# Performance work log

Hardware: AMD Instinct MI355X
Metric: run time of the kernel (lower is better)

The kernel has to match this reference:

```python
import jax, jax.numpy as jnp
import numpy as np

H = 2048   # hidden_size
NH = 32    # n_head
HS = 64    # head_size
B, T = 2, 4096
D_DECAY, D_AAA, D_MV, D_GATE = 96, 96, 64, 256


def setup_inputs() -> dict:
    key = jax.random.key(0)
    ks = jax.random.split(key, 30)
    rn = lambda k, s, sc=0.02: jax.random.normal(k, s, jnp.float32) * sc
    d = {}
    d['x'] = jax.random.normal(ks[0], (B, T, H), jnp.float32)
    d['shift_state_in'] = jax.random.normal(ks[1], (B, H), jnp.float32)
    d['wkv_state_in'] = jnp.zeros((B, NH, HS, HS), jnp.float32)
    d['v_first_val'] = jax.random.normal(ks[2], (B, T, H), jnp.float32)
    for i, n in enumerate(['x_r', 'x_w', 'x_k', 'x_v', 'x_a', 'x_g']):
        d[n] = jax.random.uniform(ks[3 + i], (H,), jnp.float32)
    d['w0'] = rn(ks[9], (H,)) - 4.0
    d['w1'] = rn(ks[10], (H, D_DECAY)); d['w2'] = rn(ks[11], (D_DECAY, H))
    d['a0'] = rn(ks[12], (H,)); d['a1'] = rn(ks[13], (H, D_AAA)); d['a2'] = rn(ks[14], (D_AAA, H))
    d['v0'] = rn(ks[15], (H,)) + 1.0; d['v1'] = rn(ks[16], (H, D_MV)); d['v2'] = rn(ks[17], (D_MV, H))
    d['g1'] = rn(ks[18], (H, D_GATE)); d['g2'] = rn(ks[19], (D_GATE, H))
    d['k_k'] = jnp.full((H,), 0.85, jnp.float32)
    d['k_a'] = jnp.ones((H,), jnp.float32)
    d['r_k'] = rn(ks[20], (NH, HS))
    s = 1.0 / np.sqrt(H)
    d['W_r'] = jax.random.normal(ks[21], (H, H), jnp.float32) * s
    d['W_k'] = jax.random.normal(ks[22], (H, H), jnp.float32) * s
    d['W_v'] = jax.random.normal(ks[23], (H, H), jnp.float32) * s
    d['W_o'] = jax.random.normal(ks[24], (H, H), jnp.float32) * s
    d['ln_w'] = jnp.ones((H,), jnp.float32)
    d['ln_b'] = jnp.zeros((H,), jnp.float32)
    return d


def _forward(x, shift_state_in, wkv_state_in, v_first_val, x_r, x_w, x_k, x_v, x_a, x_g,
             w0, w1, w2, a0, a1, a2, v0, v1, v2, g1, g2, k_k, k_a, r_k,
             W_r, W_k, W_v, W_o, ln_w, ln_b):
    Bx, Tx, C = x.shape
    # token shift: previous token embedding (shift_state for t=0)
    xprev = jnp.concatenate([shift_state_in[:, None, :], x[:, :-1]], axis=1)
    dx = xprev - x
    xr, xw, xk, xv, xa, xg = (x + dx * m for m in (x_r, x_w, x_k, x_v, x_a, x_g))
    r = xr @ W_r.T
    k = xk @ W_k.T
    v = xv @ W_v.T
    # soft-clamped log-decay (<= -0.5)
    w_raw = -jax.nn.softplus(-(w0 + jnp.tanh(xw @ w1) @ w2)) - 0.5
    # layer_id > 0: residual mix with first-layer value
    v = v + (v_first_val - v) * jax.nn.sigmoid(v0 + (xv @ v1) @ v2)
    a = jax.nn.sigmoid(a0 + (xa @ a1) @ a2)          # in-context learning rate
    g = jax.nn.sigmoid(xg @ g1) @ g2                 # output gate
    kk = (k * k_k).reshape(Bx, Tx, NH, HS)
    kk = kk / jnp.maximum(jnp.linalg.norm(kk, axis=-1, keepdims=True), 1e-12)  # F.normalize
    kk = kk.reshape(Bx, Tx, C)
    k = k * (1.0 + (a - 1.0) * k_a)
    w = jnp.exp(-jnp.exp(w_raw))                     # per-channel decay in (0,1)
    heads = lambda t: t.reshape(Bx, Tx, NH, HS).transpose(1, 0, 2, 3)  # [T,B,NH,HS]
    rs, ws, ks_, vs, kks, as_ = map(heads, (r, w, k, v, kk, a))

    def step(S, inp):
        # S: [B,NH,HS(value),HS(key)]
        rt, wt, kt, vt, kkt, at = inp
        sa = jnp.einsum('bhvk,bhk->bhv', S, -kkt)
        S = (S * wt[:, :, None, :]
             + sa[:, :, :, None] * (kkt * at)[:, :, None, :]
             + vt[:, :, :, None] * kt[:, :, None, :])
        return S, jnp.einsum('bhvk,bhk->bhv', S, rt)

    wkv_state_out, y = jax.lax.scan(step, wkv_state_in, (rs, ws, ks_, vs, kks, as_))
    y = y.transpose(1, 0, 2, 3)                      # [B,T,NH,HS]
    # GroupNorm(n_head groups, eps=1e-5*head_size)
    mu = y.mean(-1, keepdims=True)
    var = y.var(-1, keepdims=True)
    y = ((y - mu) / jnp.sqrt(var + 1e-5 * HS)).reshape(Bx, Tx, C) * ln_w + ln_b
    rk = (r.reshape(Bx, Tx, NH, HS) * k.reshape(Bx, Tx, NH, HS) * r_k).sum(-1, keepdims=True)
    y = y + (rk * v.reshape(Bx, Tx, NH, HS)).reshape(Bx, Tx, C)
    out = (y * g) @ W_o.T
    return out, x[:, -1], wkv_state_out, v_first_val


def reference(x, shift_state_in, wkv_state_in, v_first_val, x_r, x_w, x_k, x_v, x_a, x_g,
              w0, w1, w2, a0, a1, a2, v0, v1, v2, g1, g2, k_k, k_a, r_k,
              W_r, W_k, W_v, W_o, ln_w, ln_b):
    return _forward(x, shift_state_in, wkv_state_in, v_first_val, x_r, x_w, x_k, x_v, x_a, x_g,
                    w0, w1, w2, a0, a1, a2, v0, v1, v2, g1, g2, k_k, k_a, r_k,
                    W_r, W_k, W_v, W_o, ln_w, ln_b)
```

## Files before the change

### kernel.cpp

```cpp
#include <hip/hip_runtime.h>

typedef unsigned short u16;
typedef __attribute__((ext_vector_type(4))) float f32x4;
typedef __attribute__((ext_vector_type(8))) __bf16 bf16x8;
typedef __attribute__((ext_vector_type(8))) unsigned short u16x8;
typedef __attribute__((ext_vector_type(4))) unsigned short u16x4;

#define DI static __device__ __forceinline__

DI float bfu2f(u16 u){ unsigned int x = ((unsigned int)u)<<16; float f; __builtin_memcpy(&f,&x,4); return f; }
DI u16 f2bfu(float f){ __bf16 h = (__bf16)f; u16 u; __builtin_memcpy(&u,&h,2); return u; }
DI float sigm(float x){ return 1.f/(1.f+expf(-x)); }

DI void gload_lds16(const void* g, void* l) {
  __builtin_amdgcn_global_load_lds(
      (const __attribute__((address_space(1))) unsigned int*)g,
      (__attribute__((address_space(3))) unsigned int*)l, 16, 0, 0);
}

template<bool OBF16>
__global__ __launch_bounds__(256) void gemm128_k(
    const u16* __restrict__ A, const u16* __restrict__ Bt,
    void* __restrict__ Cp, int M, int N, int K)
{
  __shared__ alignas(16) u16 As[128*64];
  __shared__ alignas(16) u16 Bs[128*64];
  const int tid = threadIdx.x;
  const int wid = tid >> 6, lane = tid & 63;
  const int wm = wid >> 1, wn = wid & 1;
  const int l15 = lane & 15, q = lane >> 4;
  const int m0 = blockIdx.x * 128, n0 = blockIdx.y * 128;
  const int sr = (wid << 3) + (lane >> 3);
  const int sc = (lane & 7) << 3;
  f32x4 acc[4][4];
  #pragma unroll
  for (int i=0;i<4;i++)
    #pragma unroll
    for (int j=0;j<4;j++) acc[i][j] = f32x4{0.f,0.f,0.f,0.f};

  char* la = (char*)As + (size_t)wid*1024;
  char* lb = (char*)Bs + (size_t)wid*1024;
  for (int k0 = 0; k0 < K; k0 += 64) {
    const u16* ga = A  + (size_t)(m0 + sr)*K + k0 + sc;
    const u16* gb = Bt + (size_t)(n0 + sr)*K + k0 + sc;
    #pragma unroll
    for (int it = 0; it < 4; ++it) {
      gload_lds16(ga + (size_t)(32*it)*K, la + it*4096);
      gload_lds16(gb + (size_t)(32*it)*K, lb + it*4096);
    }
    __syncthreads();
    #pragma unroll
    for (int ks = 0; ks < 64; ks += 32) {
      bf16x8 af[4], bfv[4];
      #pragma unroll
      for (int i=0;i<4;i++) af[i]  = *(const bf16x8*)&As[(wm*64 + i*16 + l15)*64 + ks + q*8];
      #pragma unroll
      for (int j=0;j<4;j++) bfv[j] = *(const bf16x8*)&Bs[(wn*64 + j*16 + l15)*64 + ks + q*8];
      #pragma unroll
      for (int i=0;i<4;i++)
        #pragma unroll
        for (int j=0;j<4;j++)
          acc[i][j] = __builtin_amdgcn_mfma_f32_16x16x32_bf16(af[i], bfv[j], acc[i][j], 0, 0, 0);
    }
    __syncthreads();
  }
  #pragma unroll
  for (int i=0;i<4;i++)
    #pragma unroll
    for (int j=0;j<4;j++)
      #pragma unroll
      for (int rr=0;rr<4;rr++) {
        const int gm = m0 + wm*64 + i*16 + q*4 + rr;
        const int gn = n0 + wn*64 + j*16 + l15;
        const size_t o = (size_t)gm * (size_t)N + gn;
        if constexpr (OBF16) ((u16*)Cp)[o] = f2bfu(acc[i][j][rr]);
        else                 ((float*)Cp)[o] = acc[i][j][rr];
      }
}

constexpr int LDW = 72;

template<bool MIX, bool WNK, bool ABF16, bool OBF16, int EPI=0>
__global__ __launch_bounds__(256) void gemm_k(
    const void* __restrict__ Ap, const float* __restrict__ dxp, const float* __restrict__ mixp,
    const float* __restrict__ Wp, void* __restrict__ Cp, int M, int N, int K)
{
  __shared__ alignas(16) __bf16 As[64*LDW];
  __shared__ alignas(16) __bf16 Bs[64*LDW];
  const int tid = threadIdx.x;
  const int m0 = blockIdx.x * 64;
  const int n0 = blockIdx.y * 64;
  const int lane = tid & 63, wid = tid >> 6;
  const int wm = wid >> 1, wn = wid & 1;
  const int l15 = lane & 15, q = lane >> 4;
  f32x4 acc[2][2] = {{{0.f,0.f,0.f,0.f},{0.f,0.f,0.f,0.f}},
                     {{0.f,0.f,0.f,0.f},{0.f,0.f,0.f,0.f}}};

  for (int k0 = 0; k0 < K; k0 += 64) {
    {
      const int kc = (tid & 7) * 8;
      const int r0 = tid >> 3;
      #pragma unroll
      for (int it = 0; it < 2; ++it) {
        const int row = r0 + 32*it;
        const size_t gmK = (size_t)(m0 + row) * (size_t)K;
        const int gk = k0 + kc;
        if constexpr (ABF16) {
          const u16* A16 = (const u16*)Ap;
          u16x8 u;
          if (gk + 7 < K) u = *(const u16x8*)(A16 + gmK + gk);
          else {
            #pragma unroll
            for (int e=0;e<8;e++) u[e] = (gk+e < K) ? A16[gmK + gk + e] : (u16)0;
          }
          *(u16x8*)&As[row*LDW + kc] = u;
        } else {
          const float* A32 = (const float*)Ap;
          float f[8];
          if (gk + 7 < K) {
            f32x4 va = *(const f32x4*)(A32 + gmK + gk);
            f32x4 vb = *(const f32x4*)(A32 + gmK + gk + 4);
            if constexpr (MIX) {
              f32x4 d0 = *(const f32x4*)(dxp + gmK + gk);
              f32x4 d1 = *(const f32x4*)(dxp + gmK + gk + 4);
              f32x4 c0 = *(const f32x4*)(mixp + gk);
              f32x4 c1 = *(const f32x4*)(mixp + gk + 4);
              va = va + d0*c0; vb = vb + d1*c1;
            }
            #pragma unroll
            for (int e=0;e<4;e++){ f[e]=va[e]; f[4+e]=vb[e]; }
          } else {
            #pragma unroll
            for (int e=0;e<8;e++){
              const int kk2 = gk+e;
              float xv = 0.f;
              if (kk2 < K) {
                xv = A32[gmK + kk2];
                if constexpr (MIX) xv = fmaf(dxp[gmK+kk2], mixp[kk2], xv);
              }
              f[e] = xv;
            }
          }
          bf16x8 v8;
          #pragma unroll
          for (int e=0;e<8;e++) v8[e] = (__bf16)f[e];
          *(bf16x8*)&As[row*LDW + kc] = v8;
        }
      }
    }
    if constexpr (WNK) {
      const int kc = (tid & 7) * 8;
      const int r0 = tid >> 3;
      #pragma unroll
      for (int it = 0; it < 2; ++it) {
        const int row = r0 + 32*it;
        const int gn = n0 + row;
        const int gk = k0 + kc;
        float f[8];
        if (gn < N && gk + 7 < K) {
          const size_t o = (size_t)gn * (size_t)K + gk;
          f32x4 va = *(const f32x4*)(Wp + o);
          f32x4 vb = *(const f32x4*)(Wp + o + 4);
          #pragma unroll
          for (int e=0;e<4;e++){ f[e]=va[e]; f[4+e]=vb[e]; }
        } else {
          #pragma unroll
          for (int e=0;e<8;e++) f[e] = (gn < N && gk+e < K) ? Wp[(size_t)gn*K + gk + e] : 0.f;
        }
        bf16x8 v8;
        #pragma unroll
        for (int e=0;e<8;e++) v8[e] = (__bf16)f[e];
        *(bf16x8*)&Bs[row*LDW + kc] = v8;
      }
    } else {
      const int nc = (tid & 15) * 4;
      const int kr = tid >> 4;
      #pragma unroll
      for (int it = 0; it < 4; ++it) {
        const int kk = kr + 16*it;
        const int gk = k0 + kk;
        f32x4 v = {0.f,0.f,0.f,0.f};
        if (gk < K) {
          const int gn = n0 + nc;
          if (gn + 3 < N) v = *(const f32x4*)(Wp + (size_t)gk*N + gn);
          else {
            #pragma unroll
            for (int e=0;e<4;e++) if (gn+e < N) v[e] = Wp[(size_t)gk*N + gn + e];
          }
        }
        #pragma unroll
        for (int e=0;e<4;e++) Bs[(nc+e)*LDW + kk] = (__bf16)v[e];
      }
    }
    __syncthreads();
    #pragma unroll
    for (int ks = 0; ks < 64; ks += 32) {
      bf16x8 af[2], bfv[2];
      #pragma unroll
      for (int i=0;i<2;i++) af[i]  = *(const bf16x8*)&As[(wm*32 + i*16 + l15)*LDW + ks + q*8];
      #pragma unroll
      for (int i=0;i<2;i++) bfv[i] = *(const bf16x8*)&Bs[(wn*32 + i*16 + l15)*LDW + ks + q*8];
      #pragma unroll
      for (int i=0;i<2;i++)
        #pragma unroll
        for (int j=0;j<2;j++)
          acc[i][j] = __builtin_amdgcn_mfma_f32_16x16x32_bf16(af[i], bfv[j], acc[i][j], 0, 0, 0);
    }
    __syncthreads();
  }
  #pragma unroll
  for (int i=0;i<2;i++) {
    #pragma unroll
    for (int j=0;j<2;j++) {
      #pragma unroll
      for (int rr=0;rr<4;rr++) {
        const int gm = m0 + wm*32 + i*16 + q*4 + rr;
        const int gn = n0 + wn*32 + j*16 + l15;
        if (gn < N) {
          const size_t o = (size_t)gm * (size_t)N + gn;
          if constexpr (EPI == 1) {
            float* C = (float*)Cp;
            const float s = sigm(mixp[gn] + acc[i][j][rr]);
            const float vG = C[o];
            C[o] = vG + (dxp[o] - vG) * s;
          } else if constexpr (OBF16) {
            ((u16*)Cp)[o] = f2bfu(acc[i][j][rr]);
          } else {
            ((float*)Cp)[o] = acc[i][j][rr];
          }
        }
      }
    }
  }
}

__global__ void mix_cast_k(const float* __restrict__ x, const float* __restrict__ shift,
    const float* __restrict__ mr, const float* __restrict__ mw, const float* __restrict__ mk,
    const float* __restrict__ mv, const float* __restrict__ ma, const float* __restrict__ mg,
    u16* __restrict__ xr_b, u16* __restrict__ xw_b, u16* __restrict__ xk_b,
    u16* __restrict__ xv_b, u16* __restrict__ xa_b, u16* __restrict__ xg_b,
    float* __restrict__ xlast, int T_, int B_)
{
  const int Hh = 2048;
  size_t e4 = (size_t)blockIdx.x*blockDim.x + threadIdx.x;
  size_t total4 = (size_t)B_*T_*Hh/4;
  if (e4 >= total4) return;
  size_t e = e4*4;
  size_t th = (size_t)T_*Hh;
  size_t b = e / th; size_t rem = e - b*th;
  int t = (int)(rem / Hh); int c = (int)(rem & (Hh-1));
  f32x4 xv4 = *(const f32x4*)(x+e);
  f32x4 xp = t ? *(const f32x4*)(x+e-Hh) : *(const f32x4*)(shift + b*Hh + c);
  f32x4 dx = xp - xv4;
  if (t == T_-1) *(f32x4*)(xlast + b*Hh + c) = xv4;
  #define EMIT(mp, dst) { \
    f32x4 mc = *(const f32x4*)(mp + c); \
    f32x4 r_ = xv4 + dx*mc; \
    u16x4 o_; \
    o_[0]=f2bfu(r_[0]); o_[1]=f2bfu(r_[1]); o_[2]=f2bfu(r_[2]); o_[3]=f2bfu(r_[3]); \
    *(u16x4*)(dst + e) = o_; }
  EMIT(mr, xr_b) EMIT(mw, xw_b) EMIT(mk, xk_b)
  EMIT(mv, xv_b) EMIT(ma, xa_b) EMIT(mg, xg_b)
  #undef EMIT
}

__global__ void castw_k(const float* __restrict__ src, u16* __restrict__ dst, long n4){
  long i = (long)blockIdx.x*blockDim.x + threadIdx.x;
  if (i < n4) {
    f32x4 v = ((const f32x4*)src)[i];
    u16x4 o; o[0]=f2bfu(v[0]); o[1]=f2bfu(v[1]); o[2]=f2bfu(v[2]); o[3]=f2bfu(v[3]);
    ((u16x4*)dst)[i] = o;
  }
}

__global__ void ew_tanh_k(u16* p, long n){
  long i = (long)blockIdx.x*blockDim.x + threadIdx.x;
  if (i < n) p[i] = f2bfu(tanhf(bfu2f(p[i])));
}
__global__ void ew_sig_k(u16* p, long n){
  long i = (long)blockIdx.x*blockDim.x + threadIdx.x;
  if (i < n) p[i] = f2bfu(sigm(bfu2f(p[i])));
}
__global__ void ew_w_k(float* p, const float* __restrict__ w0, long n){
  long i = (long)blockIdx.x*blockDim.x + threadIdx.x;
  if (i < n) {
    int c = (int)(i & 2047);
    float z = -(w0[c] + p[i]);
    float sp = (z > 20.f) ? z : log1pf(expf(z));
    p[i] = expf(-expf(-sp - 0.5f));
  }
}
__global__ void ew_a_k(u16* p, const float* __restrict__ a0, long n){
  long i = (long)blockIdx.x*blockDim.x + threadIdx.x;
  if (i < n) { int c = (int)(i & 2047); p[i] = f2bfu(sigm(a0[c] + bfu2f(p[i]))); }
}
__global__ void copy4_k(float* __restrict__ dst, const float* __restrict__ src, long n4){
  long i = (long)blockIdx.x*blockDim.x + threadIdx.x;
  if (i < n4) ((f32x4*)dst)[i] = ((const f32x4*)src)[i];
}

__global__ __launch_bounds__(256) void rnorm_k(
    const u16* __restrict__ kb, const float* __restrict__ kkw, float* __restrict__ r2)
{
  const size_t bt = blockIdx.x;
  const int tid = threadIdx.x;
  const int c0 = tid << 3;
  u16x8 kv8 = *(const u16x8*)(kb + bt*2048 + c0);
  f32x4 ka_ = *(const f32x4*)(kkw + c0);
  f32x4 kb_ = *(const f32x4*)(kkw + c0 + 4);
  float s = 0.f;
  #pragma unroll
  for (int e=0;e<4;e++){ float kk = bfu2f(kv8[e])*ka_[e];   s = fmaf(kk,kk,s); }
  #pragma unroll
  for (int e=0;e<4;e++){ float kk = bfu2f(kv8[4+e])*kb_[e]; s = fmaf(kk,kk,s); }
  s += __shfl_xor(s, 1, 64);
  s += __shfl_xor(s, 2, 64);
  s += __shfl_xor(s, 4, 64);
  if ((tid & 7) == 0) r2[bt*32 + (tid>>3)] = 1.f/fmaxf(s, 1e-24f);
}

__global__ __launch_bounds__(64) __attribute__((amdgpu_waves_per_eu(1, 4)))
void scan_k(
    const u16* __restrict__ rb, const float* __restrict__ wb, const u16* __restrict__ kb,
    const float* __restrict__ vb, const u16* __restrict__ ab,
    const float* __restrict__ kkw, const float* __restrict__ kaw,
    const float* __restrict__ S0, float* __restrict__ yb, float* __restrict__ Sout, int T_)
{
  const int Hh = 2048, NHl = 32;
  const int blk = blockIdx.x;
  const int b = blk >> 5, h = blk & 31;
  const int lane = threadIdx.x;
  float S[64];
  const size_t sbase = (((size_t)b*NHl + h)*64 + lane)*64;
  #pragma unroll
  for (int i=0;i<64;i++) S[i] = S0[sbase+i];
  const float kkc = kkw[h*64+lane], kac = kaw[h*64+lane];
  __shared__ alignas(16) float lw[64], lkk[64], lka[64], lke[64], lr[64];
  size_t idx = (size_t)b*T_*Hh + (size_t)h*64 + lane;
  float rv = bfu2f(rb[idx]), wv = wb[idx], kv = bfu2f(kb[idx]), vv = vb[idx], av = bfu2f(ab[idx]);
  for (int t=0; t<T_; ++t) {
    float kk = kv * kkc;
    float ssum = kk*kk;
    #pragma unroll
    for (int m=1;m<64;m<<=1) ssum += __shfl_xor(ssum, m, 64);
    float inv = 1.f / fmaxf(sqrtf(ssum), 1e-12f);
    float kkn = kk * inv;
    float ke  = kv * (1.f + (av - 1.f)*kac);
    lw[lane]=wv; lkk[lane]=kkn; lka[lane]=kkn*av; lke[lane]=ke; lr[lane]=rv;
    const float vt = vv;
    __syncthreads();
    float nrv=0.f,nwv=0.f,nkv=0.f,nvv=0.f,nav=0.f;
    if (t+1 < T_) {
      const size_t ni = idx + Hh;
      nrv = bfu2f(rb[ni]); nwv = wb[ni]; nkv = bfu2f(kb[ni]); nvv = vb[ni]; nav = bfu2f(ab[ni]);
    }
    const f32x4* KK4 = (const f32x4*)lkk;
    const f32x4* W4  = (const f32x4*)lw;
    const f32x4* KA4 = (const f32x4*)lka;
    const f32x4* KE4 = (const f32x4*)lke;
    const f32x4* R4  = (const f32x4*)lr;
    float sa0=0.f,sa1=0.f,sa2=0.f,sa3=0.f;
    #pragma unroll
    for (int qq=0;qq<16;qq++){
      f32x4 k4 = KK4[qq];
      sa0 = fmaf(S[4*qq+0], k4[0], sa0);
      sa1 = fmaf(S[4*qq+1], k4[1], sa1);
      sa2 = fmaf(S[4*qq+2], k4[2], sa2);
      sa3 = fmaf(S[4*qq+3], k4[3], sa3);
    }
    const float sa = -((sa0+sa1)+(sa2+sa3));
    float y0=0.f,y1=0.f,y2=0.f,y3=0.f;
    #pragma unroll
    for (int qq=0;qq<16;qq++){
      f32x4 w4=W4[qq], a4=KA4[qq], e4=KE4[qq], r4=R4[qq];
      float s_;
      s_ = fmaf(vt, e4[0], fmaf(sa, a4[0], S[4*qq+0]*w4[0])); S[4*qq+0]=s_; y0 = fmaf(s_, r4[0], y0);
      s_ = fmaf(vt, e4[1], fmaf(sa, a4[1], S[4*qq+1]*w4[1])); S[4*qq+1]=s_; y1 = fmaf(s_, r4[1], y1);
      s_ = fmaf(vt, e4[2], fmaf(sa, a4[2], S[4*qq+2]*w4[2])); S[4*qq+2]=s_; y2 = fmaf(s_, r4[2], y2);
      s_ = fmaf(vt, e4[3], fmaf(sa, a4[3], S[4*qq+3]*w4[3])); S[4*qq+3]=s_; y3 = fmaf(s_, r4[3], y3);
    }
    yb[idx] = (y0+y1)+(y2+y3);
    __syncthreads();
    rv=nrv; wv=nwv; kv=nkv; vv=nvv; av=nav;
    idx += Hh;
  }
  #pragma unroll
  for (int i=0;i<64;i++) Sout[sbase+i] = S[i];
}

__global__ __launch_bounds__(256) void chunk_mu_k(
    const u16* __restrict__ rb, const float* __restrict__ wb, const u16* __restrict__ kb,
    const float* __restrict__ vb, const u16* __restrict__ ab,
    const float* __restrict__ kkw, const float* __restrict__ kaw,
    const float* __restrict__ r2b,
    float* __restrict__ Mbuf, float* __restrict__ Ubuf, float* __restrict__ Dbuf,
    float* __restrict__ yb, int T_, int NC)
{
  const int wid  = threadIdx.x >> 6;
  const int lane = threadIdx.x & 63;
  const int g    = blockIdx.x * 4 + wid;
  const int ch   = g >> 1;
  const bool mrole = ((g & 1) == 0);
  const int c  = ch % NC;
  const int bh = ch / NC;
  const int b = bh >> 5, h = bh & 31;

  float S[64];
  #pragma unroll
  for (int i=0;i<64;i++) S[i] = (mrole && lane == i) ? 1.f : 0.f;

  const int hc = h*64 + lane;
  const float kkc = kkw[hc], kac = kaw[hc];

  __shared__ alignas(16) float LB[4][2][5][64];
  float (*Lw)[5][64] = LB[wid];

  size_t idx = ((size_t)b*T_ + (size_t)c*64)*2048 + hc;
  size_t r2i = ((size_t)b*T_ + (size_t)c*64)*32 + h;
  float* dD = Dbuf + (size_t)ch*4096 + lane;

  {
    const float kv = bfu2f(kb[idx]);
    const float av = bfu2f(ab[idx]);
    const float kk = kv*kkc;
    Lw[0][0][lane] = wb[idx];
    Lw[0][1][lane] = kk;
    Lw[0][2][lane] = kk*av;
    Lw[0][3][lane] = kv*(1.f+(av-1.f)*kac);
    Lw[0][4][lane] = bfu2f(rb[idx]);
  }
  float vv = mrole ? 0.f : vb[idx];
  float r2 = r2b[r2i];

  for (int j=0; j<64; ++j) {
    const int cur = j & 1;
    float nr=0.f,nk=0.f,nw=0.f,na=0.f,nv=0.f,nr2=0.f;
    if (j+1 < 64) {
      const size_t ni = idx + 2048;
      nr = bfu2f(rb[ni]); nk = bfu2f(kb[ni]); nw = wb[ni]; na = bfu2f(ab[ni]);
      if (!mrole) nv = vb[ni];
      nr2 = r2b[r2i + 32];
    }
    const f32x4* W4  = (const f32x4*)Lw[cur][0];
    const f32x4* KK4 = (const f32x4*)Lw[cur][1];
    const f32x4* KA4 = (const f32x4*)Lw[cur][2];
    const f32x4* KE4 = (const f32x4*)Lw[cur][3];
    const f32x4* R4  = (const f32x4*)Lw[cur][4];
    float s0=0.f,s1=0.f,s2=0.f,s3=0.f;
    #pragma unroll
    for (int qq=0;qq<16;qq++){
      f32x4 k4 = KK4[qq];
      s0 = fmaf(S[4*qq+0], k4[0], s0);
      s1 = fmaf(S[4*qq+1], k4[1], s1);
      s2 = fmaf(S[4*qq+2], k4[2], s2);
      s3 = fmaf(S[4*qq+3], k4[3], s3);
    }
    const float sa = -((s0+s1)+(s2+s3)) * r2;
    const float vt = vv;
    float y0=0.f,y1=0.f,y2=0.f,y3=0.f;
    if (mrole) {
      #pragma unroll
      for (int qq=0;qq<16;qq++){
        f32x4 w4=W4[qq], a4=KA4[qq], r4=R4[qq];
        float s_;
        s_ = fmaf(sa, a4[0], S[4*qq+0]*w4[0]); S[4*qq+0]=s_; y0 = fmaf(s_, r4[0], y0);
        s_ = fmaf(sa, a4[1], S[4*qq+1]*w4[1]); S[4*qq+1]=s_; y1 = fmaf(s_, r4[1], y1);
        s_ = fmaf(sa, a4[2], S[4*qq+2]*w4[2]); S[4*qq+2]=s_; y2 = fmaf(s_, r4[2], y2);
        s_ = fmaf(sa, a4[3], S[4*qq+3]*w4[3]); S[4*qq+3]=s_; y3 = fmaf(s_, r4[3], y3);
      }
      dD[(size_t)j*64] = (y0+y1)+(y2+y3);
    } else {
      #pragma unroll
      for (int qq=0;qq<16;qq++){
        f32x4 w4=W4[qq], a4=KA4[qq], e4=KE4[qq], r4=R4[qq];
        float s_;
        s_ = fmaf(vt, e4[0], fmaf(sa, a4[0], S[4*qq+0]*w4[0])); S[4*qq+0]=s_; y0 = fmaf(s_, r4[0], y0);
        s_ = fmaf(vt, e4[1], fmaf(sa, a4[1], S[4*qq+1]*w4[1])); S[4*qq+1]=s_; y1 = fmaf(s_, r4[1], y1);
        s_ = fmaf(vt, e4[2], fmaf(sa, a4[2], S[4*qq+2]*w4[2])); S[4*qq+2]=s_; y2 = fmaf(s_, r4[2], y2);
        s_ = fmaf(vt, e4[3], fmaf(sa, a4[3], S[4*qq+3]*w4[3])); S[4*qq+3]=s_; y3 = fmaf(s_, r4[3], y3);
      }
      yb[idx] = (y0+y1)+(y2+y3);
    }
    if (j+1 < 64) {
      const float kk = nk*kkc;
      Lw[cur^1][0][lane] = nw;
      Lw[cur^1][1][lane] = kk;
      Lw[cur^1][2][lane] = kk*na;
      Lw[cur^1][3][lane] = nk*(1.f+(na-1.f)*kac);
      Lw[cur^1][4][lane] = nr;
    }
    vv = nv; r2 = nr2;
    idx += 2048; r2i += 32;
  }
  float* fd = (mrole ? Mbuf : Ubuf) + (size_t)ch*4096 + (size_t)lane*64;
  #pragma unroll
  for (int qq=0;qq<16;qq++)
    *(f32x4*)(fd + 4*qq) = f32x4{S[4*qq+0],S[4*qq+1],S[4*qq+2],S[4*qq+3]};
}

__global__ __launch_bounds__(256) void propagate_k(
    const float* __restrict__ Mbuf, const float* Ubuf,
    const float* __restrict__ S0, float* SSbuf, float* __restrict__ Sout, int NC)
{
  const int bh   = blockIdx.x >> 2;
  const int v0r  = (blockIdx.x & 3) * 16;
  const int tid  = threadIdx.x;
  const int lane = tid & 63;
  const int wvv  = tid >> 6;

  __shared__ float MT[64*65];
  __shared__ float Srow[16][64];

  #pragma unroll
  for (int i=0;i<4;i++) {
    const int v = v0r + wvv*4 + i;
    Srow[wvv*4+i][lane] = S0[((size_t)bh*64 + v)*64 + lane];
  }

  const size_t mbase = (size_t)bh * NC * 4096;
  f32x4 mreg[4];
  #pragma unroll
  for (int it=0; it<4; ++it)
    mreg[it] = *(const f32x4*)(Mbuf + mbase + it*1024 + tid*4);

  for (int c=0; c<NC; ++c) {
    const size_t chB = mbase + (size_t)c*4096;
    #pragma unroll
    for (int it=0; it<4; ++it) {
      const int base = it*1024 + tid*4;
      const int j = base >> 6;
      const int k = base & 63;
      #pragma unroll
      for (int e=0;e<4;e++) MT[(k+e)*65 + j] = mreg[it][e];
    }
    __syncthreads();
    if (c+1 < NC) {
      #pragma unroll
      for (int it=0; it<4; ++it)
        mreg[it] = *(const f32x4*)(Mbuf + chB + 4096 + it*1024 + tid*4);
    }
    float u[4];
    #pragma unroll
    for (int i=0;i<4;i++)
      u[i] = Ubuf[chB + (size_t)(v0r + wvv*4 + i)*64 + lane];
    #pragma unroll
    for (int i=0;i<4;i++)
      SSbuf[chB + (size_t)(v0r + wvv*4 + i)*64 + lane] = Srow[wvv*4+i][lane];
    float acc[4] = {0.f,0.f,0.f,0.f};
    #pragma unroll
    for (int j4=0; j4<16; ++j4) {
      float m0_ = MT[lane*65 + j4*4 + 0];
      float m1_ = MT[lane*65 + j4*4 + 1];
      float m2_ = MT[lane*65 + j4*4 + 2];
      float m3_ = MT[lane*65 + j4*4 + 3];
      #pragma unroll
      for (int i=0;i<4;i++) {
        f32x4 s4 = *(const f32x4*)&Srow[wvv*4+i][j4*4];
        acc[i] = fmaf(s4[0], m0_, acc[i]);
        acc[i] = fmaf(s4[1], m1_, acc[i]);
        acc[i] = fmaf(s4[2], m2_, acc[i]);
        acc[i] = fmaf(s4[3], m3_, acc[i]);
      }
    }
    #pragma unroll
    for (int i=0;i<4;i++) Srow[wvv*4+i][lane] = acc[i] + u[i];
    __syncthreads();
  }
  #pragma unroll
  for (int i=0;i<4;i++) {
    const int v = v0r + wvv*4 + i;
    Sout[((size_t)bh*64 + v)*64 + lane] = Srow[wvv*4+i][lane];
  }
}

__global__ __launch_bounds__(64) void ycorr_k(
    const float* __restrict__ SSbuf, const float* __restrict__ Dbuf,
    float* __restrict__ yb, int T_, int NC)
{
  const int ch = blockIdx.x;
  const int c  = ch % NC;
  const int bh = ch / NC;
  const int b = bh >> 5, h = bh & 31;
  const int lane = threadIdx.x;

  __shared__ alignas(16) float Dl[64*68];

  {
    const float* sg = SSbuf + (size_t)ch*4096;
    #pragma unroll
    for (int i=0;i<16;i++){
      const int o = i*256 + lane*4;
      f32x4 v = *(const f32x4*)(sg + o);
      *(f32x4*)&Dl[(o>>6)*68 + (o&63)] = v;
    }
  }
  __syncthreads();
  float ss[64];
  #pragma unroll
  for (int qq=0;qq<16;qq++){
    f32x4 v = *(const f32x4*)&Dl[lane*68 + 4*qq];
    ss[4*qq+0]=v[0]; ss[4*qq+1]=v[1]; ss[4*qq+2]=v[2]; ss[4*qq+3]=v[3];
  }
  __syncthreads();
  {
    const float* dg = Dbuf + (size_t)ch*4096;
    #pragma unroll
    for (int i=0;i<16;i++){
      const int o = i*256 + lane*4;
      f32x4 v = *(const f32x4*)(dg + o);
      *(f32x4*)&Dl[(o>>6)*68 + (o&63)] = v;
    }
  }
  __syncthreads();

  size_t idx = ((size_t)b*T_ + (size_t)c*64)*2048 + (size_t)h*64 + lane;
  for (int t=0; t<64; ++t) {
    const f32x4* D4 = (const f32x4*)&Dl[t*68];
    float a0=0.f,a1=0.f,a2=0.f,a3=0.f;
    #pragma unroll
    for (int qq=0;qq<16;qq++){
      f32x4 d4 = D4[qq];
      a0 = fmaf(ss[4*qq+0], d4[0], a0);
      a1 = fmaf(ss[4*qq+1], d4[1], a1);
      a2 = fmaf(ss[4*qq+2], d4[2], a2);
      a3 = fmaf(ss[4*qq+3], d4[3], a3);
    }
    yb[idx] = yb[idx] + ((a0+a1)+(a2+a3));
    idx += 2048;
  }
}

__global__ __launch_bounds__(256) void post_k(
    const float* __restrict__ yb, const u16* __restrict__ rb, const u16* __restrict__ kb,
    const u16* __restrict__ ab, const u16* __restrict__ gb, const float* __restrict__ vb,
    const float* __restrict__ kaw, const float* __restrict__ rkw,
    const float* __restrict__ lnw, const float* __restrict__ lnb, u16* __restrict__ zb)
{
  const int wid = threadIdx.x >> 6, lane = threadIdx.x & 63;
  const size_t unit = (size_t)blockIdx.x*4 + wid;
  const size_t bt = unit >> 5; const int h = (int)(unit & 31);
  const size_t idx = bt*2048 + (size_t)h*64 + lane;
  const int hc = h*64 + lane;
  const float yv = yb[idx];
  const float rv = bfu2f(rb[idx]), kv = bfu2f(kb[idx]), av = bfu2f(ab[idx]);
  const float ke = kv*(1.f + (av-1.f)*kaw[hc]);
  float s1 = yv, s2 = yv*yv, rk = rv*ke*rkw[hc];
  #pragma unroll
  for (int m=1;m<64;m<<=1){
    s1 += __shfl_xor(s1,m,64);
    s2 += __shfl_xor(s2,m,64);
    rk += __shfl_xor(rk,m,64);
  }
  const float mean = s1 * (1.f/64.f);
  const float var  = s2 * (1.f/64.f) - mean*mean;
  const float rstd = rsqrtf(var + 6.4e-4f);
  const float zn = (yv-mean)*rstd*lnw[hc] + lnb[hc] + rk*vb[idx];
  zb[idx] = f2bfu(zn * bfu2f(gb[idx]));
}

extern "C" void kernel_launch(void* const* d_in, const int* in_sizes, int n_in,
                              void* d_out, int out_size, void* d_ws, size_t ws_size,
                              hipStream_t stream)
{
  const float* x      = (const float*)d_in[0];
  const float* shift  = (const float*)d_in[1];
  const float* wkv0   = (const float*)d_in[2];
  const float* vfirst = (const float*)d_in[3];
  const float* xr = (const float*)d_in[4];
  const float* xw = (const float*)d_in[5];
  const float* xk = (const float*)d_in[6];
  const float* xv = (const float*)d_in[7];
  const float* xa = (const float*)d_in[8];
  const float* xg = (const float*)d_in[9];
  const float* w0 = (const float*)d_in[10];
  const float* w1 = (const float*)d_in[11];
  const float* w2 = (const float*)d_in[12];
  const float* a0 = (const float*)d_in[13];
  const float* a1 = (const float*)d_in[14];
  const float* a2 = (const float*)d_in[15];
  const float* v0 = (const float*)d_in[16];
  const float* v1 = (const float*)d_in[17];
  const float* v2 = (const float*)d_in[18];
  const float* g1 = (const float*)d_in[19];
  const float* g2 = (const float*)d_in[20];
  const float* k_k = (const float*)d_in[21];
  const float* k_a = (const float*)d_in[22];
  const float* r_k = (const float*)d_in[23];
  const float* W_r = (const float*)d_in[24];
  const float* W_k = (const float*)d_in[25];
  const float* W_v = (const float*)d_in[26];
  const float* W_o = (const float*)d_in[27];
  const float* ln_w = (const float*)d_in[28];
  const float* ln_b = (const float*)d_in[29];

  const int H = 2048, NH = 32;
  const int BH = in_sizes[1];
  const int B  = BH / H;
  const long BTH = (long)in_sizes[0];
  const int T  = (int)(BTH / BH);
  const int M  = (int)(BTH / H);

  float* out0 = (float*)d_out;
  float* out1 = out0 + BTH;
  float* out2 = out1 + BH;
  float* out3 = out2 + (size_t)B*NH*64*64;

  char* ws = (char*)d_ws;
  u16* mixb = (u16*)ws;  ws += (size_t)BTH*12;
  u16* xr_b = mixb + 0*BTH;
  u16* xw_b = mixb + 1*BTH;
  u16* xk_b = mixb + 2*BTH;
  u16* xv_b = mixb + 3*BTH;
  u16* xa_b = mixb + 4*BTH;
  u16* xg_b = mixb + 5*BTH;
  float* Mbuf  = (float*)mixb;
  float* Ubuf  = Mbuf + BTH;
  float* Dbuf  = Ubuf + BTH;
  float* SSbuf = Ubuf;
  u16*   zb16  = (u16*)mixb;
  u16* rb   = (u16*)ws;  ws += BTH*2;
  u16* kb   = (u16*)ws;  ws += BTH*2;
  u16* ab   = (u16*)ws;  ws += BTH*2;
  u16* gb   = (u16*)ws;  ws += BTH*2;
  u16* wr16 = (u16*)ws;  ws += (size_t)H*H*2;
  u16* wk16 = (u16*)ws;  ws += (size_t)H*H*2;
  u16* wv16 = (u16*)ws;  ws += (size_t)H*H*2;
  u16* wo16 = (u16*)ws;  ws += (size_t)H*H*2;
  u16* h1w  = (u16*)ws;  ws += (size_t)M*96*2;
  u16* h1a  = (u16*)ws;  ws += (size_t)M*96*2;
  u16* h1v  = (u16*)ws;  ws += (size_t)M*64*2;
  u16* h1g  = (u16*)ws;  ws += (size_t)M*256*2;
  float* dxz = (float*)ws; ws += BTH*4;
  float* r2b = (float*)h1w;
  const size_t ws_need = (size_t)(ws - (char*)d_ws);
  const bool chunked = (ws_size >= ws_need) && (T % 64 == 0);
  const bool big_ok  = (M % 128 == 0);
  (void)n_in; (void)out_size;

  const dim3 blk(256);
  auto gg  = [&](int N){ return dim3(M/64, (N+63)/64); };
  auto gg128 = [&](int N){ return dim3(M/128, N/128); };

  mix_cast_k<<<dim3((unsigned)((BTH/4 + 255)/256)), blk, 0, stream>>>(
      x, shift, xr, xw, xk, xv, xa, xg, xr_b, xw_b, xk_b, xv_b, xa_b, xg_b, out1, T, B);

  {
    const long n4 = (long)H*H/4;
    const dim3 gw((unsigned)((n4 + 255)/256));
    castw_k<<<gw, blk, 0, stream>>>(W_r, wr16, n4);
    castw_k<<<gw, blk, 0, stream>>>(W_k, wk16, n4);
    castw_k<<<gw, blk, 0, stream>>>(W_v, wv16, n4);
    castw_k<<<gw, blk, 0, stream>>>(W_o, wo16, n4);
  }

  gemm_k<false,false,true,true><<<gg(96),  blk, 0, stream>>>(xw_b, nullptr, nullptr, w1, h1w, M, 96,  H);
  gemm_k<false,false,true,true><<<gg(96),  blk, 0, stream>>>(xa_b, nullptr, nullptr, a1, h1a, M, 96,  H);
  gemm_k<false,false,true,true><<<gg(64),  blk, 0, stream>>>(xv_b, nullptr, nullptr, v1, h1v, M, 64,  H);
  gemm_k<false,false,true,true><<<gg(256), blk, 0, stream>>>(xg_b, nullptr, nullptr, g1, h1g, M, 256, H);

  ew_tanh_k<<<dim3((unsigned)(((long)M*96 + 255)/256)),  blk, 0, stream>>>(h1w, (long)M*96);
  ew_sig_k <<<dim3((unsigned)(((long)M*256 + 255)/256)), blk, 0, stream>>>(h1g, (long)M*256);

  if (big_ok) {
    gemm128_k<true ><<<gg128(H), blk, 0, stream>>>(xr_b, wr16, rb,   M, H, H);
    gemm128_k<true ><<<gg128(H), blk, 0, stream>>>(xk_b, wk16, kb,   M, H, H);
    gemm128_k<false><<<gg128(H), blk, 0, stream>>>(xv_b, wv16, out3, M, H, H);
  } else {
    gemm_k<false,true,true,true ><<<gg(H), blk, 0, stream>>>(xr_b, nullptr, nullptr, W_r, rb,   M, H, H);
    gemm_k<false,true,true,true ><<<gg(H), blk, 0, stream>>>(xk_b, nullptr, nullptr, W_k, kb,   M, H, H);
    gemm_k<false,true,true,false><<<gg(H), blk, 0, stream>>>(xv_b, nullptr, nullptr, W_v, out3, M, H, H);
  }

  gemm_k<false,false,true,false  ><<<gg(H), blk, 0, stream>>>(h1w, nullptr, nullptr, w2, dxz, M, H, 96);
  rnorm_k<<<dim3((unsigned)M), blk, 0, stream>>>(kb, k_k, r2b);
  gemm_k<false,false,true,true   ><<<gg(H), blk, 0, stream>>>(h1a, nullptr, nullptr, a2, ab,  M, H, 96);
  gemm_k<false,false,true,false,1><<<gg(H), blk, 0, stream>>>(h1v, vfirst,  v0,      v2, out3, M, H, 64);
  gemm_k<false,false,true,true   ><<<gg(H), blk, 0, stream>>>(h1g, nullptr, nullptr, g2, gb,  M, H, 256);

  const unsigned nbB = (unsigned)((BTH + 255)/256);
  ew_w_k<<<dim3(nbB), blk, 0, stream>>>(dxz, w0, BTH);
  ew_a_k<<<dim3(nbB), blk, 0, stream>>>(ab, a0, BTH);

  if (chunked) {
    const int NC = T / 64;
    const int CH = B * NH * NC;
    chunk_mu_k <<<dim3((unsigned)(2*CH/4)), blk, 0, stream>>>(rb, dxz, kb, out3, ab, k_k, k_a, r2b,
                                                              Mbuf, Ubuf, Dbuf, out0, T, NC);
    propagate_k<<<dim3(B*NH*4), blk,       0, stream>>>(Mbuf, Ubuf, wkv0, SSbuf, out2, NC);
    ycorr_k    <<<dim3(CH),     dim3(64),  0, stream>>>(SSbuf, Dbuf, out0, T, NC);
  } else {
    scan_k<<<dim3(B*NH), dim3(64), 0, stream>>>(rb, dxz, kb, out3, ab, k_k, k_a, wkv0, out0, out2, T);
  }

  post_k<<<dim3((unsigned)((size_t)M*NH/4)), blk, 0, stream>>>(out0, rb, kb, ab, gb, out3,
                                                               k_a, r_k, ln_w, ln_b, zb16);

  copy4_k<<<dim3((unsigned)((BTH/4 + 255)/256)), blk, 0, stream>>>(out3, vfirst, BTH/4);

  if (big_ok) {
    gemm128_k<false><<<gg128(H), blk, 0, stream>>>(zb16, wo16, out0, M, H, H);
  } else {
    gemm_k<false,true,true,false><<<gg(H), blk, 0, stream>>>(zb16, nullptr, nullptr, W_o, out0, M, H, H);
  }
}
```

Baseline: 1.956 ms.

## Fuse elementwise activations into GEMM epilogues and triple-buffer chunk scan LDS

Moves the tanh, sigmoid, decay-exp and a-sigmoid elementwise passes into the epilogues of the LoRA GEMMs, removing four separate kernels and their full read/write passes over large intermediate buffers. The chunked scan kernel now uses three LDS buffers and prefetches two timesteps ahead, writing the next step's LDS values before the current step's compute. It also splits the S·kk reduction into more independent accumulators. Fusing the work adds transcendental math to the GEMM epilogues. Writing LDS earlier relies on the three-buffer rotation to avoid a hazard, and the deeper prefetch raises register pressure.

After: 1.893 ms. -3.2%, faster.

```diff
diff --git a/kernel.cpp b/kernel.cpp
--- a/kernel.cpp
+++ b/kernel.cpp
@@ -218,15 +218,26 @@
         const int gn = n0 + wn*32 + j*16 + l15;
         if (gn < N) {
           const size_t o = (size_t)gm * (size_t)N + gn;
+          const float a = acc[i][j][rr];
           if constexpr (EPI == 1) {
             float* C = (float*)Cp;
-            const float s = sigm(mixp[gn] + acc[i][j][rr]);
+            const float s = sigm(mixp[gn] + a);
             const float vG = C[o];
             C[o] = vG + (dxp[o] - vG) * s;
+          } else if constexpr (EPI == 2) {
+            const float z = -(mixp[gn] + a);
+            const float sp = (z > 20.f) ? z : log1pf(expf(z));
+            ((float*)Cp)[o] = expf(-expf(-sp - 0.5f));
+          } else if constexpr (EPI == 3) {
+            ((u16*)Cp)[o] = f2bfu(sigm(mixp[gn] + a));
+          } else if constexpr (EPI == 4) {
+            ((u16*)Cp)[o] = f2bfu(tanhf(a));
+          } else if constexpr (EPI == 5) {
+            ((u16*)Cp)[o] = f2bfu(sigm(a));
           } else if constexpr (OBF16) {
-            ((u16*)Cp)[o] = f2bfu(acc[i][j][rr]);
+            ((u16*)Cp)[o] = f2bfu(a);
           } else {
-            ((float*)Cp)[o] = acc[i][j][rr];
+            ((float*)Cp)[o] = a;
           }
         }
       }
@@ -273,27 +284,6 @@
   }
 }
 
-__global__ void ew_tanh_k(u16* p, long n){
-  long i = (long)blockIdx.x*blockDim.x + threadIdx.x;
-  if (i < n) p[i] = f2bfu(tanhf(bfu2f(p[i])));
-}
-__global__ void ew_sig_k(u16* p, long n){
-  long i = (long)blockIdx.x*blockDim.x + threadIdx.x;
-  if (i < n) p[i] = f2bfu(sigm(bfu2f(p[i])));
-}
-__global__ void ew_w_k(float* p, const float* __restrict__ w0, long n){
-  long i = (long)blockIdx.x*blockDim.x + threadIdx.x;
-  if (i < n) {
-    int c = (int)(i & 2047);
-    float z = -(w0[c] + p[i]);
-    float sp = (z > 20.f) ? z : log1pf(expf(z));
-    p[i] = expf(-expf(-sp - 0.5f));
-  }
-}
-__global__ void ew_a_k(u16* p, const float* __restrict__ a0, long n){
-  long i = (long)blockIdx.x*blockDim.x + threadIdx.x;
-  if (i < n) { int c = (int)(i & 2047); p[i] = f2bfu(sigm(a0[c] + bfu2f(p[i]))); }
-}
 __global__ void copy4_k(float* __restrict__ dst, const float* __restrict__ src, long n4){
   long i = (long)blockIdx.x*blockDim.x + threadIdx.x;
   if (i < n4) ((f32x4*)dst)[i] = ((const f32x4*)src)[i];
@@ -412,7 +402,7 @@
   const int hc = h*64 + lane;
   const float kkc = kkw[hc], kac = kaw[hc];
 
-  __shared__ alignas(16) float LB[4][2][5][64];
+  __shared__ alignas(16) float LB[4][3][5][64];
   float (*Lw)[5][64] = LB[wid];
 
   size_t idx = ((size_t)b*T_ + (size_t)c*64)*2048 + hc;
@@ -429,34 +419,56 @@
     Lw[0][3][lane] = kv*(1.f+(av-1.f)*kac);
     Lw[0][4][lane] = bfu2f(rb[idx]);
   }
-  float vv = mrole ? 0.f : vb[idx];
-  float r2 = r2b[r2i];
-
+  float c_vv = mrole ? 0.f : vb[idx];
+  float c_r2 = r2b[r2i];
+  float p_r, p_k, p_w, p_a, p_v = 0.f, p_r2;
+  {
+    const size_t ni = idx + 2048;
+    p_r = bfu2f(rb[ni]); p_k = bfu2f(kb[ni]); p_w = wb[ni]; p_a = bfu2f(ab[ni]);
+    if (!mrole) p_v = vb[ni];
+    p_r2 = r2b[r2i + 32];
+  }
+
+  int cur = 0;
   for (int j=0; j<64; ++j) {
-    const int cur = j & 1;
-    float nr=0.f,nk=0.f,nw=0.f,na=0.f,nv=0.f,nr2=0.f;
+    int nxt = cur + 1; if (nxt == 3) nxt = 0;
     if (j+1 < 64) {
-      const size_t ni = idx + 2048;
-      nr = bfu2f(rb[ni]); nk = bfu2f(kb[ni]); nw = wb[ni]; na = bfu2f(ab[ni]);
-      if (!mrole) nv = vb[ni];
-      nr2 = r2b[r2i + 32];
+      const float kk = p_k*kkc;
+      Lw[nxt][0][lane] = p_w;
+      Lw[nxt][1][lane] = kk;
+      Lw[nxt][2][lane] = kk*p_a;
+      Lw[nxt][3][lane] = p_k*(1.f+(p_a-1.f)*kac);
+      Lw[nxt][4][lane] = p_r;
+    }
+    const float n_vv = p_v, n_r2 = p_r2;
+    float q_r=0.f,q_k=0.f,q_w=0.f,q_a=0.f,q_v=0.f,q_r2=0.f;
+    if (j+2 < 64) {
+      const size_t ni = idx + 4096;
+      q_r = bfu2f(rb[ni]); q_k = bfu2f(kb[ni]); q_w = wb[ni]; q_a = bfu2f(ab[ni]);
+      if (!mrole) q_v = vb[ni];
+      q_r2 = r2b[r2i + 64];
     }
     const f32x4* W4  = (const f32x4*)Lw[cur][0];
     const f32x4* KK4 = (const f32x4*)Lw[cur][1];
     const f32x4* KA4 = (const f32x4*)Lw[cur][2];
     const f32x4* KE4 = (const f32x4*)Lw[cur][3];
     const f32x4* R4  = (const f32x4*)Lw[cur][4];
-    float s0=0.f,s1=0.f,s2=0.f,s3=0.f;
-    #pragma unroll
-    for (int qq=0;qq<16;qq++){
-      f32x4 k4 = KK4[qq];
-      s0 = fmaf(S[4*qq+0], k4[0], s0);
-      s1 = fmaf(S[4*qq+1], k4[1], s1);
-      s2 = fmaf(S[4*qq+2], k4[2], s2);
-      s3 = fmaf(S[4*qq+3], k4[3], s3);
-    }
-    const float sa = -((s0+s1)+(s2+s3)) * r2;
-    const float vt = vv;
+    float sA0=0.f,sA1=0.f,sA2=0.f,sA3=0.f,sB0=0.f,sB1=0.f,sB2=0.f,sB3=0.f;
+    #pragma unroll
+    for (int qq=0;qq<8;qq++){
+      f32x4 kA = KK4[qq];
+      sA0 = fmaf(S[4*qq+0], kA[0], sA0);
+      sA1 = fmaf(S[4*qq+1], kA[1], sA1);
+      sA2 = fmaf(S[4*qq+2], kA[2], sA2);
+      sA3 = fmaf(S[4*qq+3], kA[3], sA3);
+      f32x4 kB = KK4[8+qq];
+      sB0 = fmaf(S[32+4*qq+0], kB[0], sB0);
+      sB1 = fmaf(S[32+4*qq+1], kB[1], sB1);
+      sB2 = fmaf(S[32+4*qq+2], kB[2], sB2);
+      sB3 = fmaf(S[32+4*qq+3], kB[3], sB3);
+    }
+    const float sa = -(((sA0+sB0)+(sA1+sB1)) + ((sA2+sB2)+(sA3+sB3))) * c_r2;
+    const float vt = c_vv;
     float y0=0.f,y1=0.f,y2=0.f,y3=0.f;
     if (mrole) {
       #pragma unroll
@@ -481,15 +493,9 @@
       }
       yb[idx] = (y0+y1)+(y2+y3);
     }
-    if (j+1 < 64) {
-      const float kk = nk*kkc;
-      Lw[cur^1][0][lane] = nw;
-      Lw[cur^1][1][lane] = kk;
-      Lw[cur^1][2][lane] = kk*na;
-      Lw[cur^1][3][lane] = nk*(1.f+(na-1.f)*kac);
-      Lw[cur^1][4][lane] = nr;
-    }
-    vv = nv; r2 = nr2;
+    cur = nxt;
+    c_vv = n_vv; c_r2 = n_r2;
+    p_r=q_r; p_k=q_k; p_w=q_w; p_a=q_a; p_v=q_v; p_r2=q_r2;
     idx += 2048; r2i += 32;
   }
   float* fd = (mrole ? Mbuf : Ubuf) + (size_t)ch*4096 + (size_t)lane*64;
@@ -753,13 +759,10 @@
     castw_k<<<gw, blk, 0, stream>>>(W_o, wo16, n4);
   }
 
-  gemm_k<false,false,true,true><<<gg(96),  blk, 0, stream>>>(xw_b, nullptr, nullptr, w1, h1w, M, 96,  H);
-  gemm_k<false,false,true,true><<<gg(96),  blk, 0, stream>>>(xa_b, nullptr, nullptr, a1, h1a, M, 96,  H);
-  gemm_k<false,false,true,true><<<gg(64),  blk, 0, stream>>>(xv_b, nullptr, nullptr, v1, h1v, M, 64,  H);
-  gemm_k<false,false,true,true><<<gg(256), blk, 0, stream>>>(xg_b, nullptr, nullptr, g1, h1g, M, 256, H);
-
-  ew_tanh_k<<<dim3((unsigned)(((long)M*96 + 255)/256)),  blk, 0, stream>>>(h1w, (long)M*96);
-  ew_sig_k <<<dim3((unsigned)(((long)M*256 + 255)/256)), blk, 0, stream>>>(h1g, (long)M*256);
+  gemm_k<false,false,true,true,4><<<gg(96),  blk, 0, stream>>>(xw_b, nullptr, nullptr, w1, h1w, M, 96,  H);
+  gemm_k<false,false,true,true  ><<<gg(96),  blk, 0, stream>>>(xa_b, nullptr, nullptr, a1, h1a, M, 96,  H);
+  gemm_k<false,false,true,true  ><<<gg(64),  blk, 0, stream>>>(xv_b, nullptr, nullptr, v1, h1v, M, 64,  H);
+  gemm_k<false,false,true,true,5><<<gg(256), blk, 0, stream>>>(xg_b, nullptr, nullptr, g1, h1g, M, 256, H);
 
   if (big_ok) {
     gemm128_k<true ><<<gg128(H), blk, 0, stream>>>(xr_b, wr16, rb,   M, H, H);
@@ -771,15 +774,11 @@
     gemm_k<false,true,true,false><<<gg(H), blk, 0, stream>>>(xv_b, nullptr, nullptr, W_v, out3, M, H, H);
   }
 
-  gemm_k<false,false,true,false  ><<<gg(H), blk, 0, stream>>>(h1w, nullptr, nullptr, w2, dxz, M, H, 96);
+  gemm_k<false,false,true,false,2><<<gg(H), blk, 0, stream>>>(h1w, nullptr, w0, w2, dxz, M, H, 96);
   rnorm_k<<<dim3((unsigned)M), blk, 0, stream>>>(kb, k_k, r2b);
-  gemm_k<false,false,true,true   ><<<gg(H), blk, 0, stream>>>(h1a, nullptr, nullptr, a2, ab,  M, H, 96);
-  gemm_k<false,false,true,false,1><<<gg(H), blk, 0, stream>>>(h1v, vfirst,  v0,      v2, out3, M, H, 64);
+  gemm_k<false,false,true,true,3 ><<<gg(H), blk, 0, stream>>>(h1a, nullptr, a0, a2, ab,  M, H, 96);
+  gemm_k<false,false,true,false,1><<<gg(H), blk, 0, stream>>>(h1v, vfirst,  v0, v2, out3, M, H, 64);
   gemm_k<false,false,true,true   ><<<gg(H), blk, 0, stream>>>(h1g, nullptr, nullptr, g2, gb,  M, H, 256);
-
-  const unsigned nbB = (unsigned)((BTH + 255)/256);
-  ew_w_k<<<dim3(nbB), blk, 0, stream>>>(dxz, w0, BTH);
-  ew_a_k<<<dim3(nbB), blk, 0, stream>>>(ab, a0, BTH);
 
   if (chunked) {
     const int NC = T / 64;
```
